# Optimization experiments

Hardware: AMD Instinct MI355X
Metric: run time of the kernel (lower is better)

## Reference

```python
import jax, jax.numpy as jnp
import numpy as np

B, F, L = 16384, 32, 64
FEAT, DOM, R = 100000, 8, 16
D_IN = F * L  # 2048
N_HIDDEN = 3  # hidden_units = [256, 128, 1]


def _p(k, shape, scale=0.05):
    return jax.random.normal(k, shape, dtype=jnp.float32) * scale


def setup_inputs() -> dict:
    key = jax.random.key(0)
    ks = jax.random.split(key, 32)
    return {
        'x': jax.random.randint(ks[0], (B, F), 0, FEAT),
        'd': jax.random.randint(ks[1], (B,), 0, DOM),
        'emb': _p(ks[2], (FEAT, L)),
        # share MLP: 2048 -> 1024 -> 512 (ReLU after each)
        'sW0': _p(ks[3], (D_IN, 1024)), 'sb0': _p(ks[4], (1024,)),
        'sW1': _p(ks[5], (1024, 512)), 'sb1': _p(ks[6], (512,)),
        # domain layer: 512 -> 256 shared kernel + per-domain LoRA
        'Dk0': _p(ks[7], (512, 256)), 'Db0': _p(ks[8], (256,)),
        'DA0': _p(ks[9], (DOM, 512, R)), 'DB0': _p(ks[10], (DOM, R, 256)), 'Dlb0': _p(ks[11], (DOM, 256)),
        # task layers: 256 -> 128 -> 1 shared kernels + per-task LoRA
        'Tk0': _p(ks[12], (256, 128)), 'Tb0': _p(ks[13], (128,)),
        'Tk1': _p(ks[14], (128, 1)), 'Tb1': _p(ks[15], (1,)),
        'TA0': _p(ks[16], (2, 256, R)), 'TB0': _p(ks[17], (2, R, 128)), 'Tlb0': _p(ks[18], (2, 128)),
        'TA1': _p(ks[19], (2, 128, R)), 'TB1': _p(ks[20], (2, R, 1)), 'Tlb1': _p(ks[21], (2, 1)),
        # gate hypernet + heads
        'gW0': _p(ks[22], (D_IN, 1024)), 'gb0': _p(ks[23], (1024,)),
        'gW1': _p(ks[24], (1024, 512)), 'gb1': _p(ks[25], (512,)),
        'h0W': _p(ks[26], (512, 4)), 'h0b': _p(ks[27], (4,)),
        'h1W': _p(ks[28], (512, 4)), 'h1b': _p(ks[29], (4,)),
    }


def _mlp2(x, W0, b0, W1, b1):
    return jax.nn.relu(jax.nn.relu(x @ W0 + b0) @ W1 + b1)


def _forward(x, d, emb, sW0, sb0, sW1, sb1, Dk0, Db0, DA0, DB0, Dlb0,
             Tk0, Tb0, Tk1, Tb1, TA0, TB0, Tlb0, TA1, TB1, Tlb1,
             gW0, gb0, gW1, gb1, h0W, h0b, h1W, h1b):
    x_emb = emb[x].reshape(x.shape[0], -1)          # (B, dnn_dim)
    x_dnn = _mlp2(x_emb, sW0, sb0, sW1, sb1)        # (B, 512)

    # ---- domain layer (i=0), k=0 -> ReLU applied ----
    share = x_dnn @ Dk0 + Db0                        # (B, 256)
    lora = jnp.einsum('bi,bir->br', x_dnn, DA0[d])   # per-sample domain LoRA gather+matmul
    lora = jnp.einsum('br,bro->bo', lora, DB0[d]) + Dlb0[d]
    d_dnn = jax.nn.relu(share + lora)                # activated
    # d_share / d_lora kept PRE-activation, as in source

    t_dnn = [d_dnn, d_dnn]
    t_share = [share, share]
    t_lora = [lora, lora]
    t_sl, t_ls = [], []
    Tk, Tb = [Tk0, Tk1], [Tb0, Tb1]
    TA, TB, Tlb = [TA0, TA1], [TB0, TB1], [Tlb0, Tlb1]

    k = 1  # shared counter, faithfully incremented per (i, t) step
    for i in range(2):
        for t in range(2):
            ds = t_dnn[t] @ Tk[i] + Tb[i]
            ss = t_share[t] @ Tk[i] + Tb[i]
            ls = t_lora[t] @ Tk[i] + Tb[i]
            t_ls.append(ls)
            A, Bm, lb = TA[i][t], TB[i][t], Tlb[i][t]
            dl = (t_dnn[t] @ A) @ Bm + lb[None, :]
            sl = (t_share[t] @ A) @ Bm + lb[None, :]
            ll = (t_lora[t] @ A) @ Bm + lb[None, :]
            t_dnn[t] = ds + dl
            t_share[t] = ss
            t_lora[t] = ll
            t_sl.append(sl)
            if k + 1 < N_HIDDEN:  # only fires at (i=0, t=0)
                t_dnn[t] = jax.nn.relu(t_dnn[t])
                t_share[t] = jax.nn.relu(t_share[t])
                t_lora[t] = jax.nn.relu(t_lora[t])
                t_sl[t] = jax.nn.relu(t_sl[t])
                t_ls[t] = jax.nn.relu(t_ls[t])
                k += 1

    # ---- gating (hypernet sees detached embedding) ----
    hyper = _mlp2(jax.lax.stop_gradient(x_emb), gW0, gb0, gW1, gb1)
    gates = [jax.nn.sigmoid(hyper @ h0W + h0b), jax.nn.sigmoid(hyper @ h1W + h1b)]

    outs = []
    for t in range(2):
        g = gates[t]
        # t_dnn/t_share/t_lora are (B,1); t_sl[t]/t_ls[t] are (B,128) from i=0 -> broadcast (B,128)
        outs.append(t_dnn[t] - g[:, 0:1] * t_share[t] - g[:, 1:2] * t_lora[t]
                    - g[:, 2:3] * t_sl[t] - g[:, 3:4] * t_ls[t])
    return jnp.stack(outs)  # (2, B, 128)


def reference(x, d, emb, sW0, sb0, sW1, sb1, Dk0, Db0, DA0, DB0, Dlb0,
              Tk0, Tb0, Tk1, Tb1, TA0, TB0, Tlb0, TA1, TB1, Tlb1,
              gW0, gb0, gW1, gb1, h0W, h0b, h1W, h1b):
    return _forward(x, d, emb, sW0, sb0, sW1, sb1, Dk0, Db0, DA0, DB0, Dlb0,
                    Tk0, Tb0, Tk1, Tb1, TA0, TB0, Tlb0, TA1, TB1, Tlb1,
                    gW0, gb0, gW1, gb1, h0W, h0b, h1W, h1b)
```

## Files before the change

### kernel.cpp

```cpp
#include <hip/hip_runtime.h>
#include <hip/hip_bf16.h>

#define BATCH 16384

typedef __attribute__((ext_vector_type(4))) float f32x4;
typedef __attribute__((ext_vector_type(8))) short bf16x8;

__device__ inline float b2f(unsigned short u) {
    union { unsigned u; float f; } c; c.u = ((unsigned)u) << 16; return c.f;
}
__device__ inline unsigned short f2b(float f) {
    __hip_bfloat16 h = __float2bfloat16(f);
    return *(unsigned short*)&h;
}

#define GLL16(g, l)                                                            \
    __builtin_amdgcn_global_load_lds(                                          \
        (const __attribute__((address_space(1))) void*)(g),                    \
        (__attribute__((address_space(3))) void*)(l), 16, 0, 0)

__global__ __launch_bounds__(256) void k_prep(
    const float* __restrict__ sW0, const float* __restrict__ gW0,
    const float* __restrict__ sW1, const float* __restrict__ gW1,
    const float* __restrict__ Dk0, const float* __restrict__ Tk0,
    const float* __restrict__ TA0,
    const float* __restrict__ sb0, const float* __restrict__ gb0,
    const float* __restrict__ sb1, const float* __restrict__ gb1,
    const float* __restrict__ Tb0, const float* __restrict__ Db0,
    const float* __restrict__ DA0, const float* __restrict__ DB0,
    const float* __restrict__ emb,
    unsigned short* __restrict__ W1t, unsigned short* __restrict__ W2cat,
    unsigned short* __restrict__ D3cat, unsigned short* __restrict__ Tcat,
    float* __restrict__ b1cat, float* __restrict__ b2cat, float* __restrict__ tb0c,
    float* __restrict__ d3bias, unsigned short* __restrict__ DB0b,
    unsigned short* __restrict__ embB)
{
    int id = blockIdx.x;
    const int tid = threadIdx.x;
    __shared__ float t[32][33];
    auto tcvt = [&](const float* src, int K, int N, unsigned short* dst,
                    int dst_off, int dst_ld, int bx, int by) {
        int k0 = by * 32, n0 = bx * 32;
        int tx = tid & 31, ty = tid >> 5;
        #pragma unroll
        for (int s = 0; s < 32; s += 8) {
            int k = k0 + ty + s, n = n0 + tx;
            t[ty + s][tx] = (k < K && n < N) ? src[(size_t)k * N + n] : 0.f;
        }
        __syncthreads();
        #pragma unroll
        for (int s = 0; s < 32; s += 8) {
            int n = n0 + ty + s, k = k0 + tx;
            if (n < N && k < K)
                dst[(size_t)(dst_off + n) * dst_ld + k] = f2b(t[tx][ty + s]);
        }
    };
    if (id < 4096) { int z = id >> 11, rem = id & 2047;
        tcvt(z ? gW0 : sW0, 2048, 1024, W1t, z * 1024, 2048, rem & 31, rem >> 5); return; }
    id -= 4096;
    if (id < 1024) { int z = id >> 9, rem = id & 511;
        tcvt(z ? gW1 : sW1, 1024, 512, W2cat, z * 512, 1024, rem & 15, rem >> 4); return; }
    id -= 1024;
    if (id < 128) { tcvt(Dk0, 512, 256, D3cat, 0, 512, id & 7, id >> 3); return; }
    id -= 128;
    if (id < 128) { int dom = id >> 4, by = id & 15;
        tcvt(DA0 + (size_t)dom * 512 * 16, 512, 16, D3cat, 256 + dom * 16, 512, 0, by); return; }
    id -= 128;
    if (id < 32)  { tcvt(Tk0, 256, 128, Tcat, 0, 256, id & 3, id >> 2); return; }
    id -= 32;
    if (id < 16)  { int z = id >> 3;
        tcvt(TA0 + z * 256 * 16, 256, 16, Tcat, 128 + z * 16, 256, 0, id & 7); return; }
    id -= 16;
    if (id < 143) {
        int i = id * 256 + tid;
        if (i < 1024)            { b1cat[i] = sb0[i]; return; }
        if (i < 2048)            { b1cat[i] = gb0[i - 1024]; return; }
        if (i < 2560)            { b2cat[i - 2048] = sb1[i - 2048]; return; }
        if (i < 3072)            { b2cat[i - 2560 + 512] = gb1[i - 2560]; return; }
        if (i < 3200)            { tb0c[i - 3072] = Tb0[i - 3072]; return; }
        if (i < 3232)            { tb0c[i - 3200 + 128] = 0.f; return; }
        if (i < 3488)            { d3bias[i - 3232] = Db0[i - 3232]; return; }
        if (i < 3616)            { d3bias[i - 3488 + 256] = 0.f; return; }
        i -= 3616;
        if (i < 32768)           { DB0b[i] = f2b(DB0[i]); return; }
        return;
    }
    id -= 143;
    {
        int e = (id * 256 + tid) * 4;
        if (e < 100000 * 64) {
            float4 v = *(const float4*)(emb + e);
            ushort4 o = { f2b(v.x), f2b(v.y), f2b(v.z), f2b(v.w) };
            *(ushort4*)(embB + e) = o;
        }
    }
}

template<int RELU, int OUTBF16, int GATHER>
__global__ __launch_bounds__(512, 2) void k_gemm256(
    const unsigned short* __restrict__ A, int lda, long Az,
    const unsigned short* __restrict__ Bt, int K, long Bz,
    const float* __restrict__ bias, int biasz,
    void* __restrict__ C, int ldc, long Cz,
    int N, const int* __restrict__ xsrc, const unsigned short* __restrict__ embB)
{
    extern __shared__ char smem_raw[];
    const int NT = K >> 6;
    const int tid  = threadIdx.x;
    const int lane = tid & 63;
    const int w    = tid >> 6;
    const int wr   = w >> 2, wc = w & 3;
    const int frow = lane & 15, kg = lane >> 4;
    const int z = blockIdx.z;
    A    += (size_t)z * Az;
    Bt   += (size_t)z * Bz;
    bias += (size_t)z * biasz;

    const int gx  = gridDim.x;
    const int nwg = gx * gridDim.y;
    const int lin = blockIdx.y * gx + blockIdx.x;
    const int qq  = nwg >> 3;
    const int swz = (lin & 7) * qq + (lin >> 3);
    const int bx = swz % gx, by = swz / gx;
    const int row0 = by * 256, col0 = bx * 256;

    const int lch = (lane & 7) ^ ((lane >> 3) & 7);
    const int isA = (lch < 4);
    const int eoBase = lch * 8;
    int rrh[4];
    const unsigned short* gsrc[4];
    #pragma unroll
    for (int h = 0; h < 4; ++h) {
        int rr = h * 64 + w * 8 + (lane >> 3);
        rrh[h] = rr;
        if (isA) gsrc[h] = GATHER ? embB : A + (size_t)(row0 + rr) * lda + lch * 8;
        else     gsrc[h] = Bt + (size_t)min(col0 + rr, N - 1) * K + (lch - 4) * 8;
    }
    const int dBase = w * 1024;

    const int pA = (kg ^ (frow & 7)) * 16;
    const int pB = ((4 + kg) ^ (frow & 7)) * 16;
    int aOff[8], bOff[4];
    #pragma unroll
    for (int m = 0; m < 8; ++m) aOff[m] = (wr * 128 + m * 16 + frow) * 128 + pA;
    #pragma unroll
    for (int n = 0; n < 4; ++n) bOff[n] = (wc * 64 + n * 16 + frow) * 128 + pB;

#define STAGE(t_, ks_, slot_) do {                                              \
        int tc_ = min((int)(t_), NT - 1);                                       \
        int o_ = tc_ * 64 + (ks_) * 32;                                         \
        char* d_ = smem_raw + (slot_) * 65536 + (ks_) * 32768 + dBase;          \
        GLL16(gsrc[0] + o_, d_);                                                \
        GLL16(gsrc[1] + o_, d_ + 8192);                                         \
        GLL16(gsrc[2] + o_, d_ + 16384);                                        \
        GLL16(gsrc[3] + o_, d_ + 24576);                                        \
    } while (0)
#define STAGEX(ix_, tcb_, ks_, slot_) do {                                      \
        char* d_ = smem_raw + (slot_) * 65536 + (ks_) * 32768 + dBase;          \
        _Pragma("unroll")                                                       \
        for (int h_ = 0; h_ < 4; ++h_) {                                        \
            const unsigned short* sa_ = embB + (size_t)(ix_)[h_] * 64           \
                                        + (ks_) * 32 + eoBase;                  \
            const unsigned short* sb2_ = gsrc[h_] + (tcb_) * 64 + (ks_) * 32;   \
            GLL16(isA ? sa_ : sb2_, d_ + h_ * 8192);                            \
        }                                                                       \
    } while (0)
#define READS(sb_, ks_) do {                                                    \
        _Pragma("unroll")                                                       \
        for (int n = 0; n < 4; ++n)                                             \
            bfr[n] = *(const bf16x8*)(smem_raw + (sb_) + (ks_) * 32768 + bOff[n]); \
        _Pragma("unroll")                                                       \
        for (int mi = 0; mi < 8; ++mi)                                          \
            afr[mi] = *(const bf16x8*)(smem_raw + (sb_) + (ks_) * 32768 + aOff[mi]); \
    } while (0)
#define MFMA32() do {                                                           \
        __builtin_amdgcn_s_setprio(1);                                          \
        _Pragma("unroll")                                                       \
        for (int mi = 0; mi < 8; ++mi)                                          \
            _Pragma("unroll")                                                   \
            for (int n = 0; n < 4; ++n)                                         \
                acc[mi][n] = __builtin_amdgcn_mfma_f32_16x16x32_bf16(           \
                    bfr[n], afr[mi], acc[mi][n], 0, 0, 0);                      \
        __builtin_amdgcn_s_setprio(0);                                          \
    } while (0)
#define VM4   asm volatile("s_waitcnt vmcnt(4)" ::: "memory")
#define VM8   asm volatile("s_waitcnt vmcnt(8)" ::: "memory")
#define BARM  asm volatile("s_barrier" ::: "memory")

    f32x4 acc[8][4] = {};
    bf16x8 afr[8], bfr[4];
    int ixc[4] = {0, 0, 0, 0};

    if (GATHER) {
        int ix0[4];
        #pragma unroll
        for (int h = 0; h < 4; ++h) ix0[h] = xsrc[(row0 + rrh[h]) * 32];
        int t1 = min(1, NT - 1);
        #pragma unroll
        for (int h = 0; h < 4; ++h) ixc[h] = xsrc[(row0 + rrh[h]) * 32 + t1];
        STAGEX(ix0, 0, 0, 0); STAGEX(ix0, 0, 1, 0);
    } else {
        STAGE(0, 0, 0); STAGE(0, 1, 0);
    }
    VM4; BARM;

    for (int t = 0; t < NT; ++t) {
        const int slot = t & 1, nslot = slot ^ 1;
        const int sb = slot * 65536;
        const int tcn = min(t + 1, NT - 1);
        int ixn[4];
        READS(sb, 0);
        if (GATHER) STAGEX(ixc, tcn, 0, nslot); else STAGE(t + 1, 0, nslot);
        if (GATHER) {
            int tc2 = min(t + 2, NT - 1);
            #pragma unroll
            for (int h = 0; h < 4; ++h) ixn[h] = xsrc[(row0 + rrh[h]) * 32 + tc2];
        }
        MFMA32();
        if (GATHER) VM8; else VM4;
        BARM;
        READS(sb, 1);
        if (GATHER) STAGEX(ixc, tcn, 1, nslot); else STAGE(t + 1, 1, nslot);
        MFMA32();
        if (GATHER) VM8; else VM4;
        BARM;
        if (GATHER) {
            #pragma unroll
            for (int h = 0; h < 4; ++h) ixc[h] = ixn[h];
        }
    }
#undef STAGE
#undef STAGEX
#undef READS
#undef MFMA32
#undef VM4
#undef VM8
#undef BARM

    #pragma unroll
    for (int m = 0; m < 8; ++m) {
        int row = row0 + wr * 128 + m * 16 + frow;
        #pragma unroll
        for (int n = 0; n < 4; ++n) {
            int col = col0 + wc * 64 + n * 16 + kg * 4;
            float4 bv = *(const float4*)(bias + col);
            float v0 = acc[m][n][0] + bv.x, v1 = acc[m][n][1] + bv.y;
            float v2 = acc[m][n][2] + bv.z, v3 = acc[m][n][3] + bv.w;
            if (RELU) {
                v0 = fmaxf(v0, 0.f); v1 = fmaxf(v1, 0.f);
                v2 = fmaxf(v2, 0.f); v3 = fmaxf(v3, 0.f);
            }
            if (OUTBF16) {
                ushort4 o = { f2b(v0), f2b(v1), f2b(v2), f2b(v3) };
                *(ushort4*)((unsigned short*)C + (size_t)z * Cz + (size_t)row * ldc + col) = o;
            } else {
                float4 o = { v0, v1, v2, v3 };
                *(float4*)((float*)C + (size_t)z * Cz + (size_t)row * ldc + col) = o;
            }
        }
    }
}

template<int RELU, int OUTBF16>
__global__ __launch_bounds__(256) void k_gemm(
    const unsigned short* __restrict__ A, int lda,
    const unsigned short* __restrict__ Bt,
    const float* __restrict__ bias,
    void* __restrict__ C, int ldc,
    int N, int K)
{
    __shared__ __align__(16) unsigned short As[128 * 32];
    __shared__ __align__(16) unsigned short Bs[128 * 32];
    const int tid  = threadIdx.x;
    const int lane = tid & 63;
    const int w    = tid >> 6;
    const int wr   = w >> 1, wc = w & 1;
    const int row0 = blockIdx.y * 128;
    const int col0 = blockIdx.x * 128;
    const int frow = lane & 15;
    const int kg   = lane >> 4;
    const int sw   = kg ^ ((frow >> 1) & 3);

    const int srow = w * 32 + (lane >> 2);
    const int csw  = (lane & 3) ^ ((lane >> 3) & 3);
    const int br0  = min(col0 + srow, N - 1);
    const int br1  = min(col0 + srow + 16, N - 1);

    const unsigned short* a0 = A  + (size_t)(row0 + srow) * lda      + csw * 8;
    const unsigned short* a1 = A  + (size_t)(row0 + srow + 16) * lda + csw * 8;
    const unsigned short* b0 = Bt + (size_t)br0 * K + csw * 8;
    const unsigned short* b1 = Bt + (size_t)br1 * K + csw * 8;
    unsigned short* lA0 = As + (w * 2 + 0) * 512;
    unsigned short* lA1 = As + (w * 2 + 1) * 512;
    unsigned short* lB0 = Bs + (w * 2 + 0) * 512;
    unsigned short* lB1 = Bs + (w * 2 + 1) * 512;

    f32x4 acc[4][4] = {};

    for (int bk = 0; bk < K; bk += 32) {
        __syncthreads();
        GLL16(a0 + bk, lA0);
        GLL16(a1 + bk, lA1);
        GLL16(b0 + bk, lB0);
        GLL16(b1 + bk, lB1);
        __syncthreads();
        bf16x8 af[4], bfr[4];
        #pragma unroll
        for (int m = 0; m < 4; ++m)
            af[m] = *(const bf16x8*)&As[(wr * 64 + m * 16 + frow) * 32 + sw * 8];
        #pragma unroll
        for (int n = 0; n < 4; ++n)
            bfr[n] = *(const bf16x8*)&Bs[(wc * 64 + n * 16 + frow) * 32 + sw * 8];
        #pragma unroll
        for (int m = 0; m < 4; ++m)
            #pragma unroll
            for (int n = 0; n < 4; ++n)
                acc[m][n] = __builtin_amdgcn_mfma_f32_16x16x32_bf16(bfr[n], af[m], acc[m][n], 0, 0, 0);
    }

    #pragma unroll
    for (int m = 0; m < 4; ++m) {
        int row = row0 + wr * 64 + m * 16 + frow;
        #pragma unroll
        for (int n = 0; n < 4; ++n) {
            int col = col0 + wc * 64 + n * 16 + kg * 4;
            if (col >= N) continue;
            float4 bv = *(const float4*)(bias + col);
            float v0 = acc[m][n][0] + bv.x, v1 = acc[m][n][1] + bv.y;
            float v2 = acc[m][n][2] + bv.z, v3 = acc[m][n][3] + bv.w;
            if (RELU) {
                v0 = fmaxf(v0, 0.f); v1 = fmaxf(v1, 0.f);
                v2 = fmaxf(v2, 0.f); v3 = fmaxf(v3, 0.f);
            }
            if (OUTBF16) {
                ushort4 o = { f2b(v0), f2b(v1), f2b(v2), f2b(v3) };
                *(ushort4*)((unsigned short*)C + (size_t)row * ldc + col) = o;
            } else {
                float4 o = { v0, v1, v2, v3 };
                *(float4*)((float*)C + (size_t)row * ldc + col) = o;
            }
        }
    }
}

__global__ __launch_bounds__(256) void k_dlora2(
    const unsigned short* __restrict__ SHV, const int* __restrict__ d,
    const unsigned short* __restrict__ DB0b, const float* __restrict__ Dlb0,
    unsigned short* __restrict__ SHARE,
    unsigned short* __restrict__ LORA, unsigned short* __restrict__ DDNN)
{
    int w = threadIdx.x >> 6, lane = threadIdx.x & 63;
    int b = blockIdx.x * 4 + w;
    int dom = d[b];
    const unsigned short* vp = SHV + (size_t)b * 384 + 256 + dom * 16;
    uint4 v0 = *(const uint4*)vp;
    uint4 v1 = *(const uint4*)(vp + 8);
    const unsigned short* pv0 = (const unsigned short*)&v0;
    const unsigned short* pv1 = (const unsigned short*)&v1;
    float v[16];
    #pragma unroll
    for (int r = 0; r < 8; ++r) { v[r] = b2f(pv0[r]); v[r + 8] = b2f(pv1[r]); }
    const unsigned short* Bp = DB0b + (size_t)dom * 16 * 256;
    const float* lbp = Dlb0 + (size_t)dom * 256;
    #pragma unroll
    for (int c = 0; c < 4; ++c) {
        int o = lane + c * 64;
        float a = lbp[o];
        #pragma unroll
        for (int r = 0; r < 16; ++r) a += v[r] * b2f(Bp[r * 256 + o]);
        unsigned short shb = SHV[(size_t)b * 384 + o];
        float sh = b2f(shb);
        SHARE[(size_t)b * 256 + o] = shb;
        LORA[(size_t)b * 256 + o] = f2b(a);
        DDNN[(size_t)b * 256 + o] = f2b(fmaxf(sh + a, 0.f));
    }
}

__global__ __launch_bounds__(256) void k_tail(
    const unsigned short* __restrict__ Yd, const unsigned short* __restrict__ Ys,
    const unsigned short* __restrict__ Yl,
    const unsigned short* __restrict__ Hyper,
    const float* __restrict__ TB0, const float* __restrict__ Tlb0,
    const float* __restrict__ Tk1, const float* __restrict__ Tb1,
    const float* __restrict__ TA1, const float* __restrict__ TB1, const float* __restrict__ Tlb1,
    const float* __restrict__ h0W, const float* __restrict__ h0b,
    const float* __restrict__ h1W, const float* __restrict__ h1b,
    float* __restrict__ out)
{
    __shared__ float sTB0[2][16][128];
    __shared__ float sTlb0[2][128];
    __shared__ float sTk1[128];
    __shared__ float sWeff[2][128];
    __shared__ float sY[4][3][160];
    const int tid = threadIdx.x;

    for (int i = tid; i < 4096; i += 256) ((float*)sTB0)[i] = TB0[i];
    if (tid < 256) ((float*)sTlb0)[tid] = Tlb0[tid];
    if (tid < 128) sTk1[tid] = Tk1[tid];
    {
        int t = tid >> 7, j = tid & 127;
        float a = 0.f;
        #pragma unroll
        for (int r = 0; r < 16; ++r) a += TA1[((size_t)t * 128 + j) * 16 + r] * TB1[t * 16 + r];
        sWeff[t][j] = a;
    }
    const unsigned short* Yp[3] = {Yd, Ys, Yl};
    int b0 = blockIdx.x * 4;
    for (int i = tid; i < 4 * 3 * 160; i += 256) {
        int s = i / 480, rem = i % 480, st = rem / 160, idx = rem % 160;
        sY[s][st][idx] = b2f(Yp[st][(size_t)(b0 + s) * 160 + idx]);
    }
    __syncthreads();

    int w = tid >> 6, lane = tid & 63;
    int b = b0 + w;
    const float* yd = sY[w][0];
    const float* ys = sY[w][1];
    const float* yl = sY[w][2];
    int j0 = lane, j1 = lane + 64;

    uint4 hraw = *(const uint4*)(Hyper + (size_t)b * 512 + lane * 8);
    const unsigned short* hp = (const unsigned short*)&hraw;
    float hv[8];
    #pragma unroll
    for (int j = 0; j < 8; ++j) hv[j] = b2f(hp[j]);

    float red[14];
    #pragma unroll
    for (int k = 0; k < 14; ++k) red[k] = 0.f;
    #pragma unroll
    for (int j = 0; j < 8; ++j) {
        float4 w0 = *(const float4*)(h0W + (size_t)(lane * 8 + j) * 4);
        float4 w1 = *(const float4*)(h1W + (size_t)(lane * 8 + j) * 4);
        red[0] += hv[j] * w0.x; red[1] += hv[j] * w0.y; red[2] += hv[j] * w0.z; red[3] += hv[j] * w0.w;
        red[4] += hv[j] * w1.x; red[5] += hv[j] * w1.y; red[6] += hv[j] * w1.z; red[7] += hv[j] * w1.w;
    }

    float SLv[2][2], LSv[2][2];
    #pragma unroll
    for (int t = 0; t < 2; ++t) {
        float lb0 = sTlb0[t][j0], lb1 = sTlb0[t][j1];
        float dl0 = lb0, dl1 = lb1, sl0 = lb0, sl1 = lb1, ll0 = lb0, ll1 = lb1;
        #pragma unroll
        for (int r = 0; r < 16; ++r) {
            float w0v = sTB0[t][r][j0], w1v = sTB0[t][r][j1];
            float ud = yd[128 + t * 16 + r];
            float us = ys[128 + t * 16 + r];
            float ul = yl[128 + t * 16 + r];
            dl0 += ud * w0v; dl1 += ud * w1v;
            sl0 += us * w0v; sl1 += us * w1v;
            ll0 += ul * w0v; ll1 += ul * w1v;
        }
        float D0 = yd[j0] + dl0, D1 = yd[j1] + dl1;
        float S0 = ys[j0],       S1 = ys[j1];
        float L0 = ll0,          L1 = ll1;
        float sl_0 = sl0, sl_1 = sl1;
        float ls_0 = yl[j0], ls_1 = yl[j1];
        if (t == 0) {
            D0 = fmaxf(D0, 0.f); D1 = fmaxf(D1, 0.f);
            S0 = fmaxf(S0, 0.f); S1 = fmaxf(S1, 0.f);
            L0 = fmaxf(L0, 0.f); L1 = fmaxf(L1, 0.f);
            sl_0 = fmaxf(sl_0, 0.f); sl_1 = fmaxf(sl_1, 0.f);
            ls_0 = fmaxf(ls_0, 0.f); ls_1 = fmaxf(ls_1, 0.f);
        }
        SLv[t][0] = sl_0; SLv[t][1] = sl_1;
        LSv[t][0] = ls_0; LSv[t][1] = ls_1;
        float we0 = sWeff[t][j0], we1 = sWeff[t][j1];
        float tk0 = sTk1[j0],     tk1v = sTk1[j1];
        red[8 + t * 3 + 0] = D0 * (tk0 + we0) + D1 * (tk1v + we1);
        red[8 + t * 3 + 1] = S0 * tk0 + S1 * tk1v;
        red[8 + t * 3 + 2] = L0 * we0 + L1 * we1;
    }

    #pragma unroll
    for (int s = 1; s < 64; s <<= 1) {
        #pragma unroll
        for (int k = 0; k < 14; ++k) red[k] += __shfl_xor(red[k], s, 64);
    }

    float Tb1v = Tb1[0];
    #pragma unroll
    for (int t = 0; t < 2; ++t) {
        float fd = red[8 + t * 3 + 0] + Tb1v + Tlb1[t];
        float fs = red[8 + t * 3 + 1] + Tb1v;
        float fl = red[8 + t * 3 + 2] + Tlb1[t];
        const float* hb = t ? h1b : h0b;
        float g0 = 1.f / (1.f + expf(-(red[t * 4 + 0] + hb[0])));
        float g1 = 1.f / (1.f + expf(-(red[t * 4 + 1] + hb[1])));
        float g2 = 1.f / (1.f + expf(-(red[t * 4 + 2] + hb[2])));
        float g3 = 1.f / (1.f + expf(-(red[t * 4 + 3] + hb[3])));
        float base = fd - g0 * fs - g1 * fl;
        size_t o = (size_t)t * BATCH * 128 + (size_t)b * 128;
        out[o + j0] = base - g2 * SLv[t][0] - g3 * LSv[t][0];
        out[o + j1] = base - g2 * SLv[t][1] - g3 * LSv[t][1];
    }
}

extern "C" void kernel_launch(void* const* d_in, const int* in_sizes, int n_in,
                              void* d_out, int out_size, void* d_ws, size_t ws_size,
                              hipStream_t stream)
{
    const int*   x    = (const int*)  d_in[0];
    const int*   dix  = (const int*)  d_in[1];
    const float* emb  = (const float*)d_in[2];
    const float* sW0  = (const float*)d_in[3];
    const float* sb0  = (const float*)d_in[4];
    const float* sW1  = (const float*)d_in[5];
    const float* sb1  = (const float*)d_in[6];
    const float* Dk0  = (const float*)d_in[7];
    const float* Db0  = (const float*)d_in[8];
    const float* DA0  = (const float*)d_in[9];
    const float* DB0  = (const float*)d_in[10];
    const float* Dlb0 = (const float*)d_in[11];
    const float* Tk0  = (const float*)d_in[12];
    const float* Tb0  = (const float*)d_in[13];
    const float* Tk1  = (const float*)d_in[14];
    const float* Tb1  = (const float*)d_in[15];
    const float* TA0  = (const float*)d_in[16];
    const float* TB0  = (const float*)d_in[17];
    const float* Tlb0 = (const float*)d_in[18];
    const float* TA1  = (const float*)d_in[19];
    const float* TB1  = (const float*)d_in[20];
    const float* Tlb1 = (const float*)d_in[21];
    const float* gW0  = (const float*)d_in[22];
    const float* gb0  = (const float*)d_in[23];
    const float* gW1  = (const float*)d_in[24];
    const float* gb1  = (const float*)d_in[25];
    const float* h0W  = (const float*)d_in[26];
    const float* h0b  = (const float*)d_in[27];
    const float* h1W  = (const float*)d_in[28];
    const float* h1b  = (const float*)d_in[29];

    hipFuncSetAttribute((const void*)k_gemm256<1, 1, 1>,
                        hipFuncAttributeMaxDynamicSharedMemorySize, 131072);
    hipFuncSetAttribute((const void*)k_gemm256<1, 1, 0>,
                        hipFuncAttributeMaxDynamicSharedMemorySize, 131072);

    char* ws = (char*)d_ws;
    size_t off = 0;
    auto alloc = [&](size_t bytes) -> void* {
        void* p = ws + off;
        off += (bytes + 255) & ~(size_t)255;
        return p;
    };
    unsigned short* W1t   = (unsigned short*)alloc((size_t)2048 * 2048 * 2);
    unsigned short* W2cat = (unsigned short*)alloc((size_t)1024 * 1024 * 2);
    unsigned short* D3cat = (unsigned short*)alloc((size_t)384 * 512 * 2);
    unsigned short* Tcat  = (unsigned short*)alloc((size_t)160 * 256 * 2);
    unsigned short* DB0b  = (unsigned short*)alloc((size_t)8 * 16 * 256 * 2);
    unsigned short* embB  = (unsigned short*)alloc((size_t)100000 * 64 * 2);
    float*          b1cat = (float*)alloc(2048 * 4);
    float*          b2cat = (float*)alloc(1024 * 4);
    float*          tb0c  = (float*)alloc(160 * 4);
    float*          d3bias= (float*)alloc(384 * 4);
    unsigned short* SHV   = (unsigned short*)alloc((size_t)BATCH * 384 * 2);
    unsigned short* Ybase = (unsigned short*)alloc((size_t)3 * BATCH * 160 * 2);
    char* regB = (char*)alloc((size_t)BATCH * 2048 * 2);
    unsigned short* Xdnn  = (unsigned short*)alloc((size_t)BATCH * 512 * 2);
    unsigned short* Hyper = (unsigned short*)alloc((size_t)BATCH * 512 * 2);

    unsigned short* Ys = Ybase;
    unsigned short* Yl = Ybase + (size_t)BATCH * 160;
    unsigned short* Yd = Ybase + (size_t)2 * BATCH * 160;
    unsigned short* Hbuf  = (unsigned short*)regB;
    unsigned short* SHARE = (unsigned short*)regB;
    unsigned short* LORA  = SHARE + (size_t)BATCH * 256;
    unsigned short* DDNN  = LORA  + (size_t)BATCH * 256;

    k_prep<<<11817, 256, 0, stream>>>(
        sW0, gW0, sW1, gW1, Dk0, Tk0, TA0,
        sb0, gb0, sb1, gb1, Tb0, Db0, DA0, DB0, emb,
        W1t, W2cat, D3cat, Tcat, b1cat, b2cat, tb0c, d3bias, DB0b, embB);

    k_gemm256<1, 1, 1><<<dim3(8, 64, 1), 512, 131072, stream>>>(
        embB, 0, 0, W1t, 2048, 0, b1cat, 0, Hbuf, 2048, 0, 2048, x, embB);
    k_gemm256<1, 1, 0><<<dim3(2, 64, 2), 512, 131072, stream>>>(
        Hbuf, 2048, 1024, W2cat, 1024, (long)512 * 1024, b2cat, 512,
        Xdnn, 512, (long)BATCH * 512, 512, nullptr, nullptr);
    k_gemm<0, 1><<<dim3(3, 128), 256, 0, stream>>>(Xdnn, 512, D3cat, d3bias, SHV, 384, 384, 512);
    k_dlora2<<<BATCH / 4, 256, 0, stream>>>(SHV, dix, DB0b, Dlb0, SHARE, LORA, DDNN);
    k_gemm<0, 1><<<dim3(2, 384), 256, 0, stream>>>(SHARE, 256, Tcat, tb0c, Ybase, 160, 160, 256);
    k_tail<<<BATCH / 4, 256, 0, stream>>>(Yd, Ys, Yl, Hyper, TB0, Tlb0, Tk1, Tb1,
                                          TA1, TB1, Tlb1, h0W, h0b, h1W, h1b, (float*)d_out);
}
```

Measured before the change: 320.5 us.

## Rework big GEMMs to 4-wave 256x128 tiles with triple-buffered K=32 pipeline

Replaces the 8-wave 256x256-tile GEMM with a 4-wave kernel using 256x128 output tiles and K-steps of 32. It cycles three LDS stages to keep two loads in flight per barrier. The gather variant now stages the row's embedding indices in LDS via async loads instead of per-thread scalar global reads. Smaller LDS footprint and blocks aim for better occupancy and fewer barriers per K, at the cost of more blocks and lower per-block reuse of A.

```diff
diff --git a/kernel.cpp b/kernel.cpp
--- a/kernel.cpp
+++ b/kernel.cpp
@@ -97,19 +97,19 @@
 }
 
 template<int RELU, int OUTBF16, int GATHER>
-__global__ __launch_bounds__(512, 2) void k_gemm256(
+__global__ __launch_bounds__(256, 2) void k_gemm4w(
     const unsigned short* __restrict__ A, int lda, long Az,
     const unsigned short* __restrict__ Bt, int K, long Bz,
     const float* __restrict__ bias, int biasz,
     void* __restrict__ C, int ldc, long Cz,
-    int N, const int* __restrict__ xsrc, const unsigned short* __restrict__ embB)
+    const int* __restrict__ xsrc, const unsigned short* __restrict__ embB)
 {
     extern __shared__ char smem_raw[];
-    const int NT = K >> 6;
+    const int NS = K >> 5;
     const int tid  = threadIdx.x;
     const int lane = tid & 63;
     const int w    = tid >> 6;
-    const int wr   = w >> 2, wc = w & 3;
+    const int wr   = w >> 1, wc = w & 1;
     const int frow = lane & 15, kg = lane >> 4;
     const int z = blockIdx.z;
     A    += (size_t)z * Az;
@@ -122,56 +122,58 @@
     const int qq  = nwg >> 3;
     const int swz = (lin & 7) * qq + (lin >> 3);
     const int bx = swz % gx, by = swz / gx;
-    const int row0 = by * 256, col0 = bx * 256;
-
-    const int lch = (lane & 7) ^ ((lane >> 3) & 7);
-    const int isA = (lch < 4);
-    const int eoBase = lch * 8;
+    const int row0 = by * 256, col0 = bx * 128;
+
+    const int lch = (tid & 3) ^ ((tid >> 3) & 3);
     int rrh[4];
-    const unsigned short* gsrc[4];
+    const unsigned short* gsrcA[4];
+    const unsigned short* gsrcB[2];
     #pragma unroll
     for (int h = 0; h < 4; ++h) {
-        int rr = h * 64 + w * 8 + (lane >> 3);
-        rrh[h] = rr;
-        if (isA) gsrc[h] = GATHER ? embB : A + (size_t)(row0 + rr) * lda + lch * 8;
-        else     gsrc[h] = Bt + (size_t)min(col0 + rr, N - 1) * K + (lch - 4) * 8;
-    }
+        rrh[h] = h * 64 + (tid >> 2);
+        gsrcA[h] = GATHER ? embB : A + (size_t)(row0 + rrh[h]) * lda + lch * 8;
+    }
+    #pragma unroll
+    for (int h = 0; h < 2; ++h)
+        gsrcB[h] = Bt + (size_t)(col0 + h * 64 + (tid >> 2)) * K + lch * 8;
     const int dBase = w * 1024;
 
-    const int pA = (kg ^ (frow & 7)) * 16;
-    const int pB = ((4 + kg) ^ (frow & 7)) * 16;
+    const int p = (kg ^ ((frow >> 1) & 3)) * 16;
     int aOff[8], bOff[4];
     #pragma unroll
-    for (int m = 0; m < 8; ++m) aOff[m] = (wr * 128 + m * 16 + frow) * 128 + pA;
-    #pragma unroll
-    for (int n = 0; n < 4; ++n) bOff[n] = (wc * 64 + n * 16 + frow) * 128 + pB;
-
-#define STAGE(t_, ks_, slot_) do {                                              \
-        int tc_ = min((int)(t_), NT - 1);                                       \
-        int o_ = tc_ * 64 + (ks_) * 32;                                         \
-        char* d_ = smem_raw + (slot_) * 65536 + (ks_) * 32768 + dBase;          \
-        GLL16(gsrc[0] + o_, d_);                                                \
-        GLL16(gsrc[1] + o_, d_ + 8192);                                         \
-        GLL16(gsrc[2] + o_, d_ + 16384);                                        \
-        GLL16(gsrc[3] + o_, d_ + 24576);                                        \
+    for (int m = 0; m < 8; ++m) aOff[m] = (wr * 128 + m * 16 + frow) * 64 + p;
+    #pragma unroll
+    for (int n = 0; n < 4; ++n) bOff[n] = 16384 + (wc * 64 + n * 16 + frow) * 64 + p;
+
+    const int* xbi = (const int*)(smem_raw + 73728);
+
+#define STAGE(s_, slot_, ix_) do {                                              \
+        int sc_ = min((int)(s_), NS - 1);                                       \
+        char* d_ = smem_raw + (slot_) * 24576 + dBase;                          \
+        if (GATHER) {                                                           \
+            int wo_ = (sc_ & 1) * 32 + lch * 8;                                 \
+            GLL16(embB + (size_t)(ix_)[0] * 64 + wo_, d_);                      \
+            GLL16(embB + (size_t)(ix_)[1] * 64 + wo_, d_ + 4096);               \
+            GLL16(embB + (size_t)(ix_)[2] * 64 + wo_, d_ + 8192);               \
+            GLL16(embB + (size_t)(ix_)[3] * 64 + wo_, d_ + 12288);              \
+        } else {                                                                \
+            int o_ = sc_ * 32;                                                  \
+            GLL16(gsrcA[0] + o_, d_);                                           \
+            GLL16(gsrcA[1] + o_, d_ + 4096);                                    \
+            GLL16(gsrcA[2] + o_, d_ + 8192);                                    \
+            GLL16(gsrcA[3] + o_, d_ + 12288);                                   \
+        }                                                                       \
+        int ob_ = min((int)(s_), NS - 1) * 32;                                  \
+        GLL16(gsrcB[0] + ob_, d_ + 16384);                                      \
+        GLL16(gsrcB[1] + ob_, d_ + 20480);                                      \
     } while (0)
-#define STAGEX(ix_, tcb_, ks_, slot_) do {                                      \
-        char* d_ = smem_raw + (slot_) * 65536 + (ks_) * 32768 + dBase;          \
-        _Pragma("unroll")                                                       \
-        for (int h_ = 0; h_ < 4; ++h_) {                                        \
-            const unsigned short* sa_ = embB + (size_t)(ix_)[h_] * 64           \
-                                        + (ks_) * 32 + eoBase;                  \
-            const unsigned short* sb2_ = gsrc[h_] + (tcb_) * 64 + (ks_) * 32;   \
-            GLL16(isA ? sa_ : sb2_, d_ + h_ * 8192);                            \
-        }                                                                       \
-    } while (0)
-#define READS(sb_, ks_) do {                                                    \
+#define READS4(sb_) do {                                                        \
         _Pragma("unroll")                                                       \
         for (int n = 0; n < 4; ++n)                                             \
-            bfr[n] = *(const bf16x8*)(smem_raw + (sb_) + (ks_) * 32768 + bOff[n]); \
+            bfr[n] = *(const bf16x8*)(smem_raw + (sb_) + bOff[n]);              \
         _Pragma("unroll")                                                       \
         for (int mi = 0; mi < 8; ++mi)                                          \
-            afr[mi] = *(const bf16x8*)(smem_raw + (sb_) + (ks_) * 32768 + aOff[mi]); \
+            afr[mi] = *(const bf16x8*)(smem_raw + (sb_) + aOff[mi]);            \
     } while (0)
 #define MFMA32() do {                                                           \
         __builtin_amdgcn_s_setprio(1);                                          \
@@ -183,58 +185,55 @@
                     bfr[n], afr[mi], acc[mi][n], 0, 0, 0);                      \
         __builtin_amdgcn_s_setprio(0);                                          \
     } while (0)
-#define VM4   asm volatile("s_waitcnt vmcnt(4)" ::: "memory")
-#define VM8   asm volatile("s_waitcnt vmcnt(8)" ::: "memory")
+#define VM6   asm volatile("s_waitcnt vmcnt(6)" ::: "memory")
 #define BARM  asm volatile("s_barrier" ::: "memory")
 
     f32x4 acc[8][4] = {};
     bf16x8 afr[8], bfr[4];
-    int ixc[4] = {0, 0, 0, 0};
 
     if (GATHER) {
+        const char* xs = (const char*)xsrc + (size_t)(row0 + tid) * 128;
+        GLL16(xs,      smem_raw + 73728 + dBase);
+        GLL16(xs + 16, smem_raw + 73728 + 4096 + dBase);
+        asm volatile("s_waitcnt vmcnt(0)" ::: "memory");
+        BARM;
         int ix0[4];
         #pragma unroll
-        for (int h = 0; h < 4; ++h) ix0[h] = xsrc[(row0 + rrh[h]) * 32];
-        int t1 = min(1, NT - 1);
-        #pragma unroll
-        for (int h = 0; h < 4; ++h) ixc[h] = xsrc[(row0 + rrh[h]) * 32 + t1];
-        STAGEX(ix0, 0, 0, 0); STAGEX(ix0, 0, 1, 0);
+        for (int h = 0; h < 4; ++h) ix0[h] = xbi[rrh[h] * 4];
+        STAGE(0, 0, ix0);
+        STAGE(1, 1, ix0);
     } else {
-        STAGE(0, 0, 0); STAGE(0, 1, 0);
-    }
-    VM4; BARM;
-
-    for (int t = 0; t < NT; ++t) {
-        const int slot = t & 1, nslot = slot ^ 1;
-        const int sb = slot * 65536;
-        const int tcn = min(t + 1, NT - 1);
+        int dum[4] = {0, 0, 0, 0};
+        STAGE(0, 0, dum);
+        STAGE(1, 1, dum);
+    }
+    VM6; BARM;
+
+    for (int t = 0; t < NS; ++t) {
+        const int slot = t % 3, dslot = (t + 2) % 3;
+        const int sb = slot * 24576;
         int ixn[4];
-        READS(sb, 0);
-        if (GATHER) STAGEX(ixc, tcn, 0, nslot); else STAGE(t + 1, 0, nslot);
         if (GATHER) {
-            int tc2 = min(t + 2, NT - 1);
+            int f2 = min(t + 2, NS - 1) >> 1;
+            int cb = ((f2 >> 2) & 1) * 1024 + (f2 & 3);
             #pragma unroll
-            for (int h = 0; h < 4; ++h) ixn[h] = xsrc[(row0 + rrh[h]) * 32 + tc2];
-        }
+            for (int h = 0; h < 4; ++h) ixn[h] = xbi[cb + rrh[h] * 4];
+        }
+        READS4(sb);
+        if (GATHER && (t & 7) == 6) {
+            int fs = min((t + 10) >> 1, 28);
+            int hh = ((t - 6) >> 3) & 1;
+            GLL16((const char*)xsrc + (size_t)(row0 + tid) * 128 + fs * 4,
+                  smem_raw + 73728 + hh * 4096 + dBase);
+        }
+        STAGE(t + 2, dslot, ixn);
         MFMA32();
-        if (GATHER) VM8; else VM4;
-        BARM;
-        READS(sb, 1);
-        if (GATHER) STAGEX(ixc, tcn, 1, nslot); else STAGE(t + 1, 1, nslot);
-        MFMA32();
-        if (GATHER) VM8; else VM4;
-        BARM;
-        if (GATHER) {
-            #pragma unroll
-            for (int h = 0; h < 4; ++h) ixc[h] = ixn[h];
-        }
+        VM6; BARM;
     }
 #undef STAGE
-#undef STAGEX
-#undef READS
+#undef READS4
 #undef MFMA32
-#undef VM4
-#undef VM8
+#undef VM6
 #undef BARM
 
     #pragma unroll
@@ -531,10 +530,10 @@
     const float* h1W  = (const float*)d_in[28];
     const float* h1b  = (const float*)d_in[29];
 
-    hipFuncSetAttribute((const void*)k_gemm256<1, 1, 1>,
-                        hipFuncAttributeMaxDynamicSharedMemorySize, 131072);
-    hipFuncSetAttribute((const void*)k_gemm256<1, 1, 0>,
-                        hipFuncAttributeMaxDynamicSharedMemorySize, 131072);
+    hipFuncSetAttribute((const void*)k_gemm4w<1, 1, 1>,
+                        hipFuncAttributeMaxDynamicSharedMemorySize, 81920);
+    hipFuncSetAttribute((const void*)k_gemm4w<1, 1, 0>,
+                        hipFuncAttributeMaxDynamicSharedMemorySize, 73728);
 
     char* ws = (char*)d_ws;
     size_t off = 0;
@@ -572,11 +571,11 @@
         sb0, gb0, sb1, gb1, Tb0, Db0, DA0, DB0, emb,
         W1t, W2cat, D3cat, Tcat, b1cat, b2cat, tb0c, d3bias, DB0b, embB);
 
-    k_gemm256<1, 1, 1><<<dim3(8, 64, 1), 512, 131072, stream>>>(
-        embB, 0, 0, W1t, 2048, 0, b1cat, 0, Hbuf, 2048, 0, 2048, x, embB);
-    k_gemm256<1, 1, 0><<<dim3(2, 64, 2), 512, 131072, stream>>>(
+    k_gemm4w<1, 1, 1><<<dim3(16, 64, 1), 256, 81920, stream>>>(
+        embB, 0, 0, W1t, 2048, 0, b1cat, 0, Hbuf, 2048, 0, x, embB);
+    k_gemm4w<1, 1, 0><<<dim3(4, 64, 2), 256, 73728, stream>>>(
         Hbuf, 2048, 1024, W2cat, 1024, (long)512 * 1024, b2cat, 512,
-        Xdnn, 512, (long)BATCH * 512, 512, nullptr, nullptr);
+        Xdnn, 512, (long)BATCH * 512, nullptr, nullptr);
     k_gemm<0, 1><<<dim3(3, 128), 256, 0, stream>>>(Xdnn, 512, D3cat, d3bias, SHV, 384, 384, 512);
     k_dlora2<<<BATCH / 4, 256, 0, stream>>>(SHV, dix, DB0b, Dlb0, SHARE, LORA, DDNN);
     k_gemm<0, 1><<<dim3(2, 384), 256, 0, stream>>>(SHARE, 256, Tcat, tb0c, Ybase, 160, 160, 256);
```

Measured after the change: 335.7 us. 1.05x slower.
